# Optimization experiments

Measured on AMD Instinct MI355X. Metric: run time of the kernel, lower is better.

Reference implementation:

```python
import jax, jax.numpy as jnp
import numpy as np

NHEAD = 16


def setup_inputs() -> dict:
    key = jax.random.key(0)
    ks = jax.random.split(key, 6)
    S, B, D = 2048, 2, 1024
    std = float(np.sqrt(6.0 / (D + D)))  # xavier_uniform bound
    inp = {
        "query": jax.random.normal(ks[0], (S, B, D), jnp.float32),
        "key": jax.random.normal(ks[1], (S, B, D), jnp.float32),
        "value": jax.random.normal(ks[2], (S, B, D), jnp.float32),
        "Wq": jax.random.uniform(ks[3], (D, D), jnp.float32, -std, std),
        "bq": jnp.ones((D,), jnp.float32),
        "Wk": jax.random.uniform(ks[4], (D, D), jnp.float32, -std, std),
        "bk": jnp.ones((D,), jnp.float32),
        "Wv": jax.random.uniform(ks[5], (D, D), jnp.float32, -std, std),
        "bv": jnp.ones((D,), jnp.float32),
    }
    return inp


def reference(query, key, value, Wq, bq, Wk, bk, Wv, bv):
    S, B, D = query.shape
    h = NHEAD
    d = D // h
    scale = jnp.asarray(d ** 0.5, query.dtype)
    # projections (nn.Linear: x @ W^T + b)
    q = (query @ Wq.T + bq).reshape(S, B, h, d)
    k = (key @ Wk.T + bk).reshape(S, B, h, d)
    v = (value @ Wv.T + bv).reshape(S, B, h, d)
    # batch_first=False path: scores [b,h,i,j], softmax over j, then AV
    scores = jnp.einsum('ibhd,jbhd->bhij', q, k) / scale
    attn = jax.nn.softmax(scores, axis=-1)
    out = jnp.einsum('bhij,jbhd->ibhd', attn, v).reshape(S, B, D)
    return out
```

## Files before the change

### kernel.cpp

```cpp
#include <hip/hip_runtime.h>
#include <hip/hip_bf16.h>

#define S_LEN 2048
#define BATCH 2
#define DMODEL 1024
#define NHEAD 16
#define HDIM 64
#define MTOT (S_LEN * BATCH)
#define QKV_ELEMS ((size_t)MTOT * DMODEL)

typedef __bf16 bf16x8 __attribute__((ext_vector_type(8)));
typedef unsigned short u16x8 __attribute__((ext_vector_type(8)));
typedef float f32x4 __attribute__((ext_vector_type(4)));
typedef float f32x16 __attribute__((ext_vector_type(16)));
typedef unsigned int u32x4 __attribute__((ext_vector_type(4)));

__device__ __forceinline__ unsigned short f2bf(float f) {
    unsigned int u = __float_as_uint(f);
    u += 0x7FFFu + ((u >> 16) & 1u);
    return (unsigned short)(u >> 16);
}

__device__ __forceinline__ unsigned int pack2(float lo, float hi) {
    __hip_bfloat162 h = __float22bfloat162_rn(make_float2(lo, hi));
    unsigned int r;
    __builtin_memcpy(&r, &h, 4);
    return r;
}

__device__ __forceinline__ void gload_lds16(const void* g, void* l) {
    __builtin_amdgcn_global_load_lds(
        (const __attribute__((address_space(1))) unsigned int*)g,
        (__attribute__((address_space(3))) unsigned int*)l, 16, 0, 0);
}

#define PBM 128
#define PBN 128
#define PBK 32
#define PLDS 48
#define QSCALE 0.18033688011112042f

__global__ __launch_bounds__(256) void proj_kernel(
        const float* __restrict__ Xq, const float* __restrict__ Xk,
        const float* __restrict__ Xv, const float* __restrict__ Wq,
        const float* __restrict__ Wk, const float* __restrict__ Wv,
        const float* __restrict__ bq, const float* __restrict__ bk,
        const float* __restrict__ bv, unsigned short* __restrict__ ws)
{
    const int work = (blockIdx.x & 7) * 96 + (blockIdx.x >> 3);
    const int t    = work >> 8;
    const int rem  = work & 255;
    const int m0   = (rem >> 3) * PBM;
    const int n0   = (rem & 7) * PBN;

    const float* X    = (t == 0) ? Xq : (t == 1) ? Xk : Xv;
    const float* W    = (t == 0) ? Wq : (t == 1) ? Wk : Wv;
    const float* bias = (t == 0) ? bq : (t == 1) ? bk : bv;
    unsigned short* out = ws + (size_t)t * QKV_ELEMS;
    const float scale = (t == 0) ? QSCALE : 1.0f;

    __shared__ __align__(16) unsigned short lds[(PBM + PBN) * PLDS];
    unsigned short* Alds = lds;
    unsigned short* Blds = lds + PBM * PLDS;

    const int tid = threadIdx.x;
    const int wave = tid >> 6;
    const int lane = tid & 63;
    const int lrow = lane & 15;
    const int lg   = lane >> 4;
    const int wr = (wave >> 1) * 64;
    const int wc = (wave & 1) * 64;

    f32x4 acc[4][4];
#pragma unroll
    for (int i = 0; i < 4; ++i)
#pragma unroll
        for (int j = 0; j < 4; ++j)
            acc[i][j] = (f32x4){0.f, 0.f, 0.f, 0.f};

    const int sr = tid >> 3;
    const int sg = tid & 7;

    for (int k0 = 0; k0 < DMODEL; k0 += PBK) {
        __syncthreads();
#pragma unroll
        for (int it = 0; it < 4; ++it) {
            const int row = sr + it * 32;
            const float4 va = *(const float4*)(X + (size_t)(m0 + row) * DMODEL + k0 + sg * 4);
            const float4 vb = *(const float4*)(W + (size_t)(n0 + row) * DMODEL + k0 + sg * 4);
            ushort4 ha, hb;
            ha.x = f2bf(va.x); ha.y = f2bf(va.y); ha.z = f2bf(va.z); ha.w = f2bf(va.w);
            hb.x = f2bf(vb.x); hb.y = f2bf(vb.y); hb.z = f2bf(vb.z); hb.w = f2bf(vb.w);
            *(ushort4*)&Alds[row * PLDS + sg * 4] = ha;
            *(ushort4*)&Blds[row * PLDS + sg * 4] = hb;
        }
        __syncthreads();

        bf16x8 af[4], bw[4];
#pragma unroll
        for (int i = 0; i < 4; ++i) {
            af[i] = *(const bf16x8*)&Alds[(wr + i * 16 + lrow) * PLDS + lg * 8];
            bw[i] = *(const bf16x8*)&Blds[(wc + i * 16 + lrow) * PLDS + lg * 8];
        }
#pragma unroll
        for (int i = 0; i < 4; ++i)
#pragma unroll
            for (int j = 0; j < 4; ++j)
                acc[i][j] = __builtin_amdgcn_mfma_f32_16x16x32_bf16(af[i], bw[j], acc[i][j], 0, 0, 0);
    }

#pragma unroll
    for (int j = 0; j < 4; ++j) {
        const int n  = n0 + wc + j * 16 + lrow;
        const float bv_ = bias[n];
        const int h  = n >> 6;
        const int dd = n & 63;
#pragma unroll
        for (int i = 0; i < 4; ++i) {
#pragma unroll
            for (int r = 0; r < 4; ++r) {
                const int m = m0 + wr + i * 16 + lg * 4 + r;
                const int s = m >> 1;
                const int b = m & 1;
                const float v = (acc[i][j][r] + bv_) * scale;
                size_t idx;
                if (t == 2)
                    idx = ((size_t)((b * NHEAD + h) * HDIM + dd)) * S_LEN + s;
                else
                    idx = ((size_t)((b * NHEAD + h) * S_LEN + s)) * HDIM + dd;
                out[idx] = f2bf(v);
            }
        }
    }
}

#define NT (S_LEN / 64)

__global__ __launch_bounds__(512) void attn_kernel(
        const unsigned short* __restrict__ ws, float* __restrict__ out)
{
    const unsigned short* Qw = ws;
    const unsigned short* Kw = ws + QKV_ELEMS;
    const unsigned short* Vw = ws + 2 * QKV_ELEMS;

    const int bid = blockIdx.x;
    const int idx = bid >> 3;
    const int bh  = (bid & 7) * 4 + (idx >> 3);
    const int q0  = (idx & 7) * 256;

    __shared__ __align__(16) unsigned short Kbuf[2][64 * 64];
    __shared__ __align__(16) unsigned short Vbuf[2][64 * 64];
    __shared__ unsigned int Pu[8][32 * 32];

    const int tid  = threadIdx.x;
    const int wave = tid >> 6;
    const int lane = tid & 63;
    const int l31  = lane & 31;
    const int half = lane >> 5;

    const size_t base = (size_t)bh * S_LEN * HDIM;
    const int qrow = q0 + wave * 32 + l31;

    bf16x8 qf[4];
#pragma unroll
    for (int c = 0; c < 4; ++c)
        qf[c] = *(const bf16x8*)(Qw + base + (size_t)qrow * HDIM + c * 16 + half * 8);

    bf16x8 ones;
    {
        u16x8 o;
#pragma unroll
        for (int e = 0; e < 8; ++e) o[e] = 0x3F80;
        ones = __builtin_bit_cast(bf16x8, o);
    }

    f32x16 Od0, Od1, Lacc;
#pragma unroll
    for (int i = 0; i < 16; ++i) { Od0[i] = 0.f; Od1[i] = 0.f; Lacc[i] = 0.f; }
    float mrun = -__builtin_inff();

    int g_[4];
#pragma unroll
    for (int c = 0; c < 4; ++c) g_[c] = ((c * 2 + half) ^ (l31 & 7)) * 8;

    const int srow = tid >> 3;
    const int sgrp = (tid & 7) ^ (srow & 7);
    const int dsto = tid * 8;

    gload_lds16(Kw + base + (size_t)srow * HDIM + sgrp * 8,  &Kbuf[0][dsto]);
    gload_lds16(Vw + base + (size_t)srow * S_LEN + sgrp * 8, &Vbuf[0][dsto]);
    __syncthreads();

    int cur = 0;
    for (int t = 0; t < NT; ++t) {
        if (t + 1 < NT) {
            const int sn = (t + 1) * 64;
            gload_lds16(Kw + base + (size_t)(sn + srow) * HDIM + sgrp * 8, &Kbuf[cur ^ 1][dsto]);
            gload_lds16(Vw + base + (size_t)srow * S_LEN + sn + sgrp * 8, &Vbuf[cur ^ 1][dsto]);
        }

        const unsigned short* Klds = Kbuf[cur];
        const unsigned short* Vlds = Vbuf[cur];

        f32x16 S0, S1;
#pragma unroll
        for (int i = 0; i < 16; ++i) { S0[i] = 0.f; S1[i] = 0.f; }
        __builtin_amdgcn_s_setprio(1);
#pragma unroll
        for (int c = 0; c < 4; ++c) {
            const bf16x8 ka0 = *(const bf16x8*)&Klds[l31 * 64 + g_[c]];
            const bf16x8 ka1 = *(const bf16x8*)&Klds[(32 + l31) * 64 + g_[c]];
            S0 = __builtin_amdgcn_mfma_f32_32x32x16_bf16(ka0, qf[c], S0, 0, 0, 0);
            S1 = __builtin_amdgcn_mfma_f32_32x32x16_bf16(ka1, qf[c], S1, 0, 0, 0);
        }
        __builtin_amdgcn_s_setprio(0);

        float m16[16];
#pragma unroll
        for (int i = 0; i < 16; ++i) m16[i] = fmaxf(S0[i], S1[i]);
        float a0 = fmaxf(fmaxf(m16[0],  m16[1]),  m16[2]);
        float a1 = fmaxf(fmaxf(m16[3],  m16[4]),  m16[5]);
        float a2 = fmaxf(fmaxf(m16[6],  m16[7]),  m16[8]);
        float a3 = fmaxf(fmaxf(m16[9],  m16[10]), m16[11]);
        float a4 = fmaxf(fmaxf(m16[12], m16[13]), m16[14]);
        float b0 = fmaxf(fmaxf(a0, a1), a2);
        float b1 = fmaxf(fmaxf(a3, a4), m16[15]);
        float mx = fmaxf(b0, b1);
        mx = fmaxf(mx, __shfl_xor(mx, 32, 64));

        if (!__all(mx - mrun <= 8.0f)) {
            const float mnew = fmaxf(mrun, mx);
            const float ex   = exp2f(mrun - mnew);
            mrun = mnew;
            Od0 *= ex;
            Od1 *= ex;
            Lacc *= ex;
        }

#pragma unroll
        for (int i = 0; i < 16; ++i) S0[i] = exp2f(S0[i] - mrun);
#pragma unroll
        for (int i = 0; i < 16; ++i) S1[i] = exp2f(S1[i] - mrun);

#pragma unroll
        for (int w = 0; w < 8; ++w) {
            const unsigned int pk0 = pack2(S0[2 * w], S0[2 * w + 1]);
            const unsigned int pk1 = pack2(S1[2 * w], S1[2 * w + 1]);
            const int kp = (w & 1) + 4 * (w >> 1) + 2 * half;
            Pu[wave][kp * 32 + l31]        = pk0;
            Pu[wave][(16 + kp) * 32 + l31] = pk1;
        }
        __asm__ volatile("" ::: "memory");

        __builtin_amdgcn_s_setprio(1);
#pragma unroll
        for (int c = 0; c < 4; ++c) {
            const bf16x8 va0 = *(const bf16x8*)&Vlds[l31 * 64 + g_[c]];
            const bf16x8 va1 = *(const bf16x8*)&Vlds[(32 + l31) * 64 + g_[c]];
            u32x4 pu;
#pragma unroll
            for (int e = 0; e < 4; ++e)
                pu[e] = Pu[wave][(c * 8 + half * 4 + e) * 32 + l31];
            const bf16x8 pb = __builtin_bit_cast(bf16x8, pu);
            Od0  = __builtin_amdgcn_mfma_f32_32x32x16_bf16(va0,  pb, Od0,  0, 0, 0);
            Od1  = __builtin_amdgcn_mfma_f32_32x32x16_bf16(va1,  pb, Od1,  0, 0, 0);
            Lacc = __builtin_amdgcn_mfma_f32_32x32x16_bf16(ones, pb, Lacc, 0, 0, 0);
        }
        __builtin_amdgcn_s_setprio(0);

        __syncthreads();
        cur ^= 1;
    }

    const int bb = bh >> 4;
    const int hh = bh & 15;
    const float inv = 1.0f / Lacc[0];
    float* op = out + (size_t)qrow * (BATCH * DMODEL) + bb * DMODEL + hh * HDIM;
#pragma unroll
    for (int gg = 0; gg < 4; ++gg) {
        const int d0 = gg * 8 + half * 4;
        float4 v0, v1;
        v0.x = Od0[gg * 4 + 0] * inv; v0.y = Od0[gg * 4 + 1] * inv;
        v0.z = Od0[gg * 4 + 2] * inv; v0.w = Od0[gg * 4 + 3] * inv;
        v1.x = Od1[gg * 4 + 0] * inv; v1.y = Od1[gg * 4 + 1] * inv;
        v1.z = Od1[gg * 4 + 2] * inv; v1.w = Od1[gg * 4 + 3] * inv;
        *(float4*)(op + d0)      = v0;
        *(float4*)(op + 32 + d0) = v1;
    }
}

extern "C" void kernel_launch(void* const* d_in, const int* in_sizes, int n_in,
                              void* d_out, int out_size, void* d_ws, size_t ws_size,
                              hipStream_t stream) {
    const float* q  = (const float*)d_in[0];
    const float* k  = (const float*)d_in[1];
    const float* v  = (const float*)d_in[2];
    const float* Wq = (const float*)d_in[3];
    const float* bq = (const float*)d_in[4];
    const float* Wk = (const float*)d_in[5];
    const float* bk = (const float*)d_in[6];
    const float* Wv = (const float*)d_in[7];
    const float* bv = (const float*)d_in[8];
    unsigned short* ws = (unsigned short*)d_ws;
    float* out = (float*)d_out;

    proj_kernel<<<dim3(768), dim3(256), 0, stream>>>(q, k, v, Wq, Wk, Wv, bq, bk, bv, ws);
    attn_kernel<<<dim3(256), dim3(512), 0, stream>>>(ws, out);
}
```

Measured before the change: 151.1 us.

## Switch attention to 16x16x32 MFMA with 16-row query tiles per wave

The attention kernel now has each wave process 16 query rows with 16x16x32 bf16 MFMAs instead of 32 rows with 32x32x16. The grid doubles to 512 blocks of 128 queries, launch bounds request 4 blocks per CU, and the P scratch buffer is padded to stride 17 to avoid LDS bank conflicts. The aim is more parallelism across CUs and lower register pressure for higher occupancy. In exchange, K/V tiles are loaded and reused across fewer query rows, which raises global and LDS traffic per FLOP.

```diff
diff --git a/kernel.cpp b/kernel.cpp
--- a/kernel.cpp
+++ b/kernel.cpp
@@ -12,7 +12,6 @@
 typedef __bf16 bf16x8 __attribute__((ext_vector_type(8)));
 typedef unsigned short u16x8 __attribute__((ext_vector_type(8)));
 typedef float f32x4 __attribute__((ext_vector_type(4)));
-typedef float f32x16 __attribute__((ext_vector_type(16)));
 typedef unsigned int u32x4 __attribute__((ext_vector_type(4)));
 
 __device__ __forceinline__ unsigned short f2bf(float f) {
@@ -135,8 +134,9 @@
 }
 
 #define NT (S_LEN / 64)
-
-__global__ __launch_bounds__(512) void attn_kernel(
+#define PUSTR 17
+
+__global__ __launch_bounds__(512, 4) void attn_kernel(
         const unsigned short* __restrict__ ws, float* __restrict__ out)
 {
     const unsigned short* Qw = ws;
@@ -145,26 +145,26 @@
 
     const int bid = blockIdx.x;
     const int idx = bid >> 3;
-    const int bh  = (bid & 7) * 4 + (idx >> 3);
-    const int q0  = (idx & 7) * 256;
+    const int bh  = (bid & 7) * 4 + (idx >> 4);
+    const int q0  = (idx & 15) * 128;
 
     __shared__ __align__(16) unsigned short Kbuf[2][64 * 64];
     __shared__ __align__(16) unsigned short Vbuf[2][64 * 64];
-    __shared__ unsigned int Pu[8][32 * 32];
+    __shared__ unsigned int Pu[8][32 * PUSTR];
 
     const int tid  = threadIdx.x;
     const int wave = tid >> 6;
     const int lane = tid & 63;
-    const int l31  = lane & 31;
-    const int half = lane >> 5;
+    const int lrow = lane & 15;
+    const int lg   = lane >> 4;
 
     const size_t base = (size_t)bh * S_LEN * HDIM;
-    const int qrow = q0 + wave * 32 + l31;
-
-    bf16x8 qf[4];
-#pragma unroll
-    for (int c = 0; c < 4; ++c)
-        qf[c] = *(const bf16x8*)(Qw + base + (size_t)qrow * HDIM + c * 16 + half * 8);
+    const int qrow = q0 + wave * 16 + lrow;
+
+    bf16x8 qf[2];
+#pragma unroll
+    for (int c = 0; c < 2; ++c)
+        qf[c] = *(const bf16x8*)(Qw + base + (size_t)qrow * HDIM + c * 32 + lg * 8);
 
     bf16x8 ones;
     {
@@ -174,14 +174,11 @@
         ones = __builtin_bit_cast(bf16x8, o);
     }
 
-    f32x16 Od0, Od1, Lacc;
-#pragma unroll
-    for (int i = 0; i < 16; ++i) { Od0[i] = 0.f; Od1[i] = 0.f; Lacc[i] = 0.f; }
+    f32x4 O[4], Lacc;
+#pragma unroll
+    for (int dt = 0; dt < 4; ++dt) O[dt] = (f32x4){0.f, 0.f, 0.f, 0.f};
+    Lacc = (f32x4){0.f, 0.f, 0.f, 0.f};
     float mrun = -__builtin_inff();
-
-    int g_[4];
-#pragma unroll
-    for (int c = 0; c < 4; ++c) g_[c] = ((c * 2 + half) ^ (l31 & 7)) * 8;
 
     const int srow = tid >> 3;
     const int sgrp = (tid & 7) ^ (srow & 7);
@@ -202,70 +199,76 @@
         const unsigned short* Klds = Kbuf[cur];
         const unsigned short* Vlds = Vbuf[cur];
 
-        f32x16 S0, S1;
-#pragma unroll
-        for (int i = 0; i < 16; ++i) { S0[i] = 0.f; S1[i] = 0.f; }
+        f32x4 S[4];
+#pragma unroll
+        for (int kt = 0; kt < 4; ++kt) S[kt] = (f32x4){0.f, 0.f, 0.f, 0.f};
         __builtin_amdgcn_s_setprio(1);
 #pragma unroll
-        for (int c = 0; c < 4; ++c) {
-            const bf16x8 ka0 = *(const bf16x8*)&Klds[l31 * 64 + g_[c]];
-            const bf16x8 ka1 = *(const bf16x8*)&Klds[(32 + l31) * 64 + g_[c]];
-            S0 = __builtin_amdgcn_mfma_f32_32x32x16_bf16(ka0, qf[c], S0, 0, 0, 0);
-            S1 = __builtin_amdgcn_mfma_f32_32x32x16_bf16(ka1, qf[c], S1, 0, 0, 0);
+        for (int kt = 0; kt < 4; ++kt) {
+#pragma unroll
+            for (int c = 0; c < 2; ++c) {
+                const int g = ((c * 4 + lg) ^ (lrow & 7)) * 8;
+                const bf16x8 ka = *(const bf16x8*)&Klds[(kt * 16 + lrow) * 64 + g];
+                S[kt] = __builtin_amdgcn_mfma_f32_16x16x32_bf16(ka, qf[c], S[kt], 0, 0, 0);
+            }
         }
         __builtin_amdgcn_s_setprio(0);
 
-        float m16[16];
-#pragma unroll
-        for (int i = 0; i < 16; ++i) m16[i] = fmaxf(S0[i], S1[i]);
-        float a0 = fmaxf(fmaxf(m16[0],  m16[1]),  m16[2]);
-        float a1 = fmaxf(fmaxf(m16[3],  m16[4]),  m16[5]);
-        float a2 = fmaxf(fmaxf(m16[6],  m16[7]),  m16[8]);
-        float a3 = fmaxf(fmaxf(m16[9],  m16[10]), m16[11]);
-        float a4 = fmaxf(fmaxf(m16[12], m16[13]), m16[14]);
-        float b0 = fmaxf(fmaxf(a0, a1), a2);
-        float b1 = fmaxf(fmaxf(a3, a4), m16[15]);
-        float mx = fmaxf(b0, b1);
+        float m0_ = fmaxf(fmaxf(S[0][0], S[0][1]), fmaxf(S[0][2], S[0][3]));
+        float m1_ = fmaxf(fmaxf(S[1][0], S[1][1]), fmaxf(S[1][2], S[1][3]));
+        float m2_ = fmaxf(fmaxf(S[2][0], S[2][1]), fmaxf(S[2][2], S[2][3]));
+        float m3_ = fmaxf(fmaxf(S[3][0], S[3][1]), fmaxf(S[3][2], S[3][3]));
+        float mx = fmaxf(fmaxf(m0_, m1_), fmaxf(m2_, m3_));
+        mx = fmaxf(mx, __shfl_xor(mx, 16, 64));
         mx = fmaxf(mx, __shfl_xor(mx, 32, 64));
 
         if (!__all(mx - mrun <= 8.0f)) {
             const float mnew = fmaxf(mrun, mx);
             const float ex   = exp2f(mrun - mnew);
             mrun = mnew;
-            Od0 *= ex;
-            Od1 *= ex;
+#pragma unroll
+            for (int dt = 0; dt < 4; ++dt) O[dt] *= ex;
             Lacc *= ex;
         }
 
 #pragma unroll
-        for (int i = 0; i < 16; ++i) S0[i] = exp2f(S0[i] - mrun);
-#pragma unroll
-        for (int i = 0; i < 16; ++i) S1[i] = exp2f(S1[i] - mrun);
-
-#pragma unroll
-        for (int w = 0; w < 8; ++w) {
-            const unsigned int pk0 = pack2(S0[2 * w], S0[2 * w + 1]);
-            const unsigned int pk1 = pack2(S1[2 * w], S1[2 * w + 1]);
-            const int kp = (w & 1) + 4 * (w >> 1) + 2 * half;
-            Pu[wave][kp * 32 + l31]        = pk0;
-            Pu[wave][(16 + kp) * 32 + l31] = pk1;
+        for (int kt = 0; kt < 4; ++kt)
+#pragma unroll
+            for (int r = 0; r < 4; ++r)
+                S[kt][r] = exp2f(S[kt][r] - mrun);
+
+#pragma unroll
+        for (int kt = 0; kt < 4; ++kt) {
+#pragma unroll
+            for (int i = 0; i < 2; ++i) {
+                const unsigned int dw = pack2(S[kt][2 * i], S[kt][2 * i + 1]);
+                const int kp = kt * 8 + lg * 2 + i;
+                Pu[wave][kp * PUSTR + lrow] = dw;
+            }
         }
         __asm__ volatile("" ::: "memory");
 
         __builtin_amdgcn_s_setprio(1);
-#pragma unroll
-        for (int c = 0; c < 4; ++c) {
-            const bf16x8 va0 = *(const bf16x8*)&Vlds[l31 * 64 + g_[c]];
-            const bf16x8 va1 = *(const bf16x8*)&Vlds[(32 + l31) * 64 + g_[c]];
+        bf16x8 pb[2];
+#pragma unroll
+        for (int c = 0; c < 2; ++c) {
             u32x4 pu;
 #pragma unroll
             for (int e = 0; e < 4; ++e)
-                pu[e] = Pu[wave][(c * 8 + half * 4 + e) * 32 + l31];
-            const bf16x8 pb = __builtin_bit_cast(bf16x8, pu);
-            Od0  = __builtin_amdgcn_mfma_f32_32x32x16_bf16(va0,  pb, Od0,  0, 0, 0);
-            Od1  = __builtin_amdgcn_mfma_f32_32x32x16_bf16(va1,  pb, Od1,  0, 0, 0);
-            Lacc = __builtin_amdgcn_mfma_f32_32x32x16_bf16(ones, pb, Lacc, 0, 0, 0);
-        }
+                pu[e] = Pu[wave][(c * 16 + lg * 4 + e) * PUSTR + lrow];
+            pb[c] = __builtin_bit_cast(bf16x8, pu);
+        }
+#pragma unroll
+        for (int dt = 0; dt < 4; ++dt) {
+#pragma unroll
+            for (int c = 0; c < 2; ++c) {
+                const int g = ((c * 4 + lg) ^ (lrow & 7)) * 8;
+                const bf16x8 va = *(const bf16x8*)&Vlds[(dt * 16 + lrow) * 64 + g];
+                O[dt] = __builtin_amdgcn_mfma_f32_16x16x32_bf16(va, pb[c], O[dt], 0, 0, 0);
+            }
+        }
+        Lacc = __builtin_amdgcn_mfma_f32_16x16x32_bf16(ones, pb[0], Lacc, 0, 0, 0);
+        Lacc = __builtin_amdgcn_mfma_f32_16x16x32_bf16(ones, pb[1], Lacc, 0, 0, 0);
         __builtin_amdgcn_s_setprio(0);
 
         __syncthreads();
@@ -277,15 +280,11 @@
     const float inv = 1.0f / Lacc[0];
     float* op = out + (size_t)qrow * (BATCH * DMODEL) + bb * DMODEL + hh * HDIM;
 #pragma unroll
-    for (int gg = 0; gg < 4; ++gg) {
-        const int d0 = gg * 8 + half * 4;
-        float4 v0, v1;
-        v0.x = Od0[gg * 4 + 0] * inv; v0.y = Od0[gg * 4 + 1] * inv;
-        v0.z = Od0[gg * 4 + 2] * inv; v0.w = Od0[gg * 4 + 3] * inv;
-        v1.x = Od1[gg * 4 + 0] * inv; v1.y = Od1[gg * 4 + 1] * inv;
-        v1.z = Od1[gg * 4 + 2] * inv; v1.w = Od1[gg * 4 + 3] * inv;
-        *(float4*)(op + d0)      = v0;
-        *(float4*)(op + 32 + d0) = v1;
+    for (int dt = 0; dt < 4; ++dt) {
+        float4 v;
+        v.x = O[dt][0] * inv; v.y = O[dt][1] * inv;
+        v.z = O[dt][2] * inv; v.w = O[dt][3] * inv;
+        *(float4*)(op + dt * 16 + lg * 4) = v;
     }
 }
 
@@ -305,5 +304,5 @@
     float* out = (float*)d_out;
 
     proj_kernel<<<dim3(768), dim3(256), 0, stream>>>(q, k, v, Wq, Wk, Wv, bq, bk, bv, ws);
-    attn_kernel<<<dim3(256), dim3(512), 0, stream>>>(ws, out);
-}
+    attn_kernel<<<dim3(512), dim3(512), 0, stream>>>(ws, out);
+}
```

New measurement: 143.4 us. -5.1%, faster.
